# Performance work log

Measured on AMD Instinct MI355X. Metric: run time of the kernel, lower is better.

## Reference

```python
import jax, jax.numpy as jnp
import numpy as np
import math

B, C, H, W, S = 8, 512, 64, 64, 4


def setup_inputs() -> dict:
    key = jax.random.key(0)
    ks = jax.random.split(key, 7)
    s = 1.0 / math.sqrt(C)  # ~ torch Linear init scale
    x = jax.random.normal(ks[0], (B, C, H, W), jnp.float32)
    Wq = jax.random.uniform(ks[1], (C, C), jnp.float32, -s, s)
    bq = jax.random.uniform(ks[2], (C,), jnp.float32, -s, s)
    Wk = jax.random.uniform(ks[3], (C, C), jnp.float32, -s, s)
    bk = jax.random.uniform(ks[4], (C,), jnp.float32, -s, s)
    Wv = jax.random.uniform(ks[5], (C, C), jnp.float32, -s, s)
    bv = jax.random.uniform(ks[6], (C,), jnp.float32, -s, s)
    return {"x": x, "Wq": Wq, "bq": bq, "Wk": Wk, "bk": bk, "Wv": Wv, "bv": bv}


def reference(x, Wq, bq, Wk, bk, Wv, bv):
    # x: (B, C, H, W). Faithful to the torch module's output, but expressed
    # in the algebraically-equivalent efficient form: the repeat_interleaved
    # attention matrix A is block-constant, so out = repeat(A_m @ Vsum).
    b, c, h, w = x.shape
    nb = (h // S) * (w // S)  # number of SxS spatial blocks
    hw = h * w
    ss = S * S

    # Block means in unfold order (bh, bw): (B, nb, C)
    x_avg = x.reshape(b, c, h // S, S, w // S, S).mean(axis=(3, 5))
    x_avg = x_avg.reshape(b, c, nb).transpose(0, 2, 1)

    Q = x_avg @ Wq.T + bq  # (B, nb, C)
    K = x_avg @ Wk.T + bk  # (B, nb, C)
    A = jax.nn.softmax(jnp.einsum('bnc,bmc->bnm', Q, K) / jnp.sqrt(jnp.float32(c)), axis=-1)

    # V over flat row-major pixels: (B, HW, C)
    x_flat = x.reshape(b, c, hw).transpose(0, 2, 1)
    V = x_flat @ Wv.T + bv

    # repeat_interleave on dim=2 means column group j of A sums V rows
    # [j*ss, (j+1)*ss) in FLAT pixel order (not spatial blocks) - faithful.
    Vsum = V.reshape(b, hw // ss, ss, c).sum(axis=2)  # (B, nb, C)
    out_small = jnp.einsum('bnm,bmc->bnc', A, Vsum)   # (B, nb, C)
    # repeat_interleave on dim=1: each block row broadcast to ss flat pixels
    out_flat = jnp.repeat(out_small, ss, axis=1)      # (B, HW, C)
    return out_flat.transpose(0, 2, 1).reshape(b, c, h, w)
```

## Files before the change

kernel.cpp:

```cpp
#include <hip/hip_runtime.h>

typedef __attribute__((ext_vector_type(8))) short short8;
typedef __attribute__((ext_vector_type(4))) float f32x4;

__device__ __forceinline__ unsigned short f2bf(float f) {
    union { float f; unsigned int i; } v; v.f = f;
    unsigned int x = v.i;
    return (unsigned short)((x + 0x7FFFu + ((x >> 16) & 1u)) >> 16);
}
__device__ __forceinline__ f32x4 mfma16(short8 a, short8 b, f32x4 c) {
    return __builtin_amdgcn_mfma_f32_16x16x32_bf16(a, b, c, 0, 0, 0);
}

__global__ void prep_kernel(const float* __restrict__ x,
                            const float* __restrict__ Wq,
                            const float* __restrict__ Wk,
                            const float* __restrict__ Wv,
                            unsigned short* __restrict__ xavg,
                            unsigned short* __restrict__ xsum,
                            unsigned short* __restrict__ Wb)
{
    const int blk = blockIdx.x;
    const int t = threadIdx.x;
    if (blk >= 4096) {
        const int f = (blk - 4096) * 512 + t;
        const int m = f >> 16;
        const int o = f & 65535;
        const float4* s4 = (const float4*)((m == 0) ? Wq : (m == 1) ? Wk : Wv);
        float4 a = s4[o];
        float4 b = s4[o + 256];
        ushort4* d4 = (ushort4*)(Wb + (size_t)m * 262144);
        d4[o]       = make_ushort4(f2bf(a.x), f2bf(a.y), f2bf(a.z), f2bf(a.w));
        d4[o + 256] = make_ushort4(f2bf(b.x), f2bf(b.y), f2bf(b.z), f2bf(b.w));
        return;
    }
    const int b = blk >> 9;
    const int c = blk & 511;

    const float4* x4 = (const float4*)(x + (size_t)blk * 4096);
    float4 f0 = x4[t], f1 = x4[t + 256], f2 = x4[t + 512], f3 = x4[t + 768];

    __shared__ float part2[1024];
    part2[t]       = f0.x + f0.y + f0.z + f0.w;
    part2[t + 256] = f1.x + f1.y + f1.z + f1.w;
    part2[t + 512] = f2.x + f2.y + f2.z + f2.w;
    part2[t + 768] = f3.x + f3.y + f3.z + f3.w;
    __syncthreads();

    {
        const int base = 16 * (t >> 2) + 4 * (t & 3);
        float4 q = *(const float4*)&part2[base];
        xsum[((size_t)b * 256 + t) * 512 + c] = f2bf(q.x + q.y + q.z + q.w);
    }
    {
        const int bh = t >> 4, bw = t & 15;
        float m = (part2[(bh * 4 + 0) * 16 + bw] + part2[(bh * 4 + 1) * 16 + bw] +
                   part2[(bh * 4 + 2) * 16 + bw] + part2[(bh * 4 + 3) * 16 + bw]) * 0.0625f;
        xavg[((size_t)b * 256 + t) * 512 + c] = f2bf(m);
    }
}

__global__ void __launch_bounds__(256, 2)
proj_gemm(const unsigned short* __restrict__ xavg,
          const unsigned short* __restrict__ xsum,
          const unsigned short* __restrict__ Wb,
          const float* __restrict__ bq,
          const float* __restrict__ bk,
          const float* __restrict__ bv,
          unsigned short* __restrict__ QK,
          unsigned short* __restrict__ VsT)
{
    const int blk = blockIdx.x;
    const int lane = threadIdx.x & 63, quad = lane >> 4, r16 = lane & 15;
    const int w = threadIdx.x >> 6;

    if (blk < 256) {
        const int wave = blk * 4 + w;
        const int mt2 = wave >> 4;
        const int nt4 = wave & 15;
        const unsigned short* xp0 = xavg + (size_t)(mt2 * 32 + r16) * 512 + quad * 8;
        const unsigned short* xp1 = xp0 + 16 * 512;
        const unsigned short* wp0 = Wb + (size_t)(nt4 * 64 + r16) * 512 + quad * 8;
        const unsigned short* wp1 = wp0 + 16 * 512;
        const unsigned short* wp2 = wp0 + 32 * 512;
        const unsigned short* wp3 = wp0 + 48 * 512;

        f32x4 a00 = {0,0,0,0}, a01 = a00, a02 = a00, a03 = a00;
        f32x4 a10 = a00, a11 = a00, a12 = a00, a13 = a00;
#pragma unroll 4
        for (int k = 0; k < 512; k += 32) {
            short8 qa0 = *(const short8*)(xp0 + k);
            short8 qa1 = *(const short8*)(xp1 + k);
            short8 b0 = *(const short8*)(wp0 + k);
            short8 b1 = *(const short8*)(wp1 + k);
            short8 b2 = *(const short8*)(wp2 + k);
            short8 b3 = *(const short8*)(wp3 + k);
            a00 = mfma16(qa0, b0, a00); a01 = mfma16(qa0, b1, a01);
            a02 = mfma16(qa0, b2, a02); a03 = mfma16(qa0, b3, a03);
            a10 = mfma16(qa1, b0, a10); a11 = mfma16(qa1, b1, a11);
            a12 = mfma16(qa1, b2, a12); a13 = mfma16(qa1, b3, a13);
        }
        const int row0 = mt2 * 32 + quad * 4;
        f32x4 accs0[4] = {a00, a01, a02, a03};
        f32x4 accs1[4] = {a10, a11, a12, a13};
#pragma unroll
        for (int j = 0; j < 4; ++j) {
            const int c = nt4 * 64 + j * 16 + r16;
            const float bias = (c < 512) ? bq[c] : bk[c - 512];
#pragma unroll
            for (int r = 0; r < 4; ++r) {
                QK[(size_t)(row0 + r) * 1024 + c]      = f2bf(accs0[j][r] + bias);
                QK[(size_t)(row0 + 16 + r) * 1024 + c] = f2bf(accs1[j][r] + bias);
            }
        }
    } else {
        const int vblk = blk - 256;
        const int b = vblk >> 4;
        const int wave = (vblk & 15) * 4 + w;
        const int mt2 = wave >> 3;
        const int nt4 = wave & 7;
        const unsigned short* xp0 = xsum + (size_t)b * 131072 + (size_t)(mt2 * 32 + r16) * 512 + quad * 8;
        const unsigned short* xp1 = xp0 + 16 * 512;
        const unsigned short* wp0 = Wb + 524288 + (size_t)(nt4 * 64 + r16) * 512 + quad * 8;
        const unsigned short* wp1 = wp0 + 16 * 512;
        const unsigned short* wp2 = wp0 + 32 * 512;
        const unsigned short* wp3 = wp0 + 48 * 512;

        f32x4 a00 = {0,0,0,0}, a01 = a00, a02 = a00, a03 = a00;
        f32x4 a10 = a00, a11 = a00, a12 = a00, a13 = a00;
#pragma unroll 4
        for (int k = 0; k < 512; k += 32) {
            short8 qa0 = *(const short8*)(xp0 + k);
            short8 qa1 = *(const short8*)(xp1 + k);
            short8 b0 = *(const short8*)(wp0 + k);
            short8 b1 = *(const short8*)(wp1 + k);
            short8 b2 = *(const short8*)(wp2 + k);
            short8 b3 = *(const short8*)(wp3 + k);
            a00 = mfma16(qa0, b0, a00); a01 = mfma16(qa0, b1, a01);
            a02 = mfma16(qa0, b2, a02); a03 = mfma16(qa0, b3, a03);
            a10 = mfma16(qa1, b0, a10); a11 = mfma16(qa1, b1, a11);
            a12 = mfma16(qa1, b2, a12); a13 = mfma16(qa1, b3, a13);
        }
        unsigned short* vb = VsT + (size_t)b * 131072;
        const int m0 = mt2 * 32 + quad * 4;
        f32x4 accs0[4] = {a00, a01, a02, a03};
        f32x4 accs1[4] = {a10, a11, a12, a13};
#pragma unroll
        for (int j = 0; j < 4; ++j) {
            const int c = nt4 * 64 + j * 16 + r16;
            const float bias = 16.f * bv[c];
#pragma unroll
            for (int r = 0; r < 4; ++r) {
                vb[(size_t)c * 256 + m0 + r]      = f2bf(accs0[j][r] + bias);
                vb[(size_t)c * 256 + m0 + 16 + r] = f2bf(accs1[j][r] + bias);
            }
        }
    }
}

__global__ void __launch_bounds__(256, 2)
score_softmax(const unsigned short* __restrict__ QK,
              unsigned short* __restrict__ Amat)
{
    __shared__ float S[16][257];
    const int b = blockIdx.y, strip = blockIdx.x;
    const int w = threadIdx.x >> 6, lane = threadIdx.x & 63;
    const int quad = lane >> 4, r16 = lane & 15;

    {
        const unsigned short* qp = QK + (size_t)(b * 256 + strip * 16 + r16) * 1024 + quad * 8;
        const unsigned short* kp0 = QK + (size_t)(b * 256 + w * 64 + r16) * 1024 + 512 + quad * 8;
        const unsigned short* kp1 = kp0 + 16 * 1024;
        const unsigned short* kp2 = kp0 + 32 * 1024;
        const unsigned short* kp3 = kp0 + 48 * 1024;

        f32x4 a0 = {0,0,0,0}, a1 = a0, a2 = a0, a3 = a0;
#pragma unroll 4
        for (int k = 0; k < 512; k += 32) {
            short8 qa = *(const short8*)(qp + k);
            short8 b0 = *(const short8*)(kp0 + k);
            short8 b1 = *(const short8*)(kp1 + k);
            short8 b2 = *(const short8*)(kp2 + k);
            short8 b3 = *(const short8*)(kp3 + k);
            a0 = mfma16(qa, b0, a0); a1 = mfma16(qa, b1, a1);
            a2 = mfma16(qa, b2, a2); a3 = mfma16(qa, b3, a3);
        }
        f32x4 accs[4] = {a0, a1, a2, a3};
#pragma unroll
        for (int j = 0; j < 4; ++j) {
            const int col = w * 64 + j * 16 + r16;
#pragma unroll
            for (int r = 0; r < 4; ++r)
                S[quad * 4 + r][col] = accs[j][r];
        }
    }
    __syncthreads();

    {
        const int t = threadIdx.x;
        const int r = t >> 4, idx = t & 15;
        float v[16];
        float mx = -3.4e38f;
#pragma unroll
        for (int j = 0; j < 16; ++j) {
            v[j] = S[r][idx * 16 + j] * 0.044194173824159216f;
            mx = fmaxf(mx, v[j]);
        }
        mx = fmaxf(mx, __shfl_xor(mx, 1));
        mx = fmaxf(mx, __shfl_xor(mx, 2));
        mx = fmaxf(mx, __shfl_xor(mx, 4));
        mx = fmaxf(mx, __shfl_xor(mx, 8));
        float sum = 0.f;
#pragma unroll
        for (int j = 0; j < 16; ++j) { v[j] = __expf(v[j] - mx); sum += v[j]; }
        sum += __shfl_xor(sum, 1);
        sum += __shfl_xor(sum, 2);
        sum += __shfl_xor(sum, 4);
        sum += __shfl_xor(sum, 8);
        const float inv = 1.f / sum;
        unsigned short* ap = Amat + (size_t)b * 65536 + (size_t)(strip * 16 + r) * 256 + idx * 16;
#pragma unroll
        for (int j = 0; j < 16; j += 4)
            *(ushort4*)(ap + j) = make_ushort4(f2bf(v[j] * inv), f2bf(v[j + 1] * inv),
                                               f2bf(v[j + 2] * inv), f2bf(v[j + 3] * inv));
    }
}

__global__ void __launch_bounds__(256, 4)
av_expand(const unsigned short* __restrict__ Amat,
          const unsigned short* __restrict__ VsT,
          float* __restrict__ out)
{
    __shared__ float osT[64][17];
    const int b = blockIdx.y;
    const int sh = blockIdx.x >> 3;
    const int cq = blockIdx.x & 7;
    const int w = threadIdx.x >> 6, lane = threadIdx.x & 63;
    const int quad = lane >> 4, r16 = lane & 15;

    {
        const unsigned short* ap = Amat + (size_t)b * 65536 + (size_t)(sh * 16 + r16) * 256 + quad * 8;
        const unsigned short* vp = VsT + (size_t)b * 131072 +
                                   (size_t)(cq * 64 + w * 16 + r16) * 256 + quad * 8;
        f32x4 acc = {0.f, 0.f, 0.f, 0.f};
#pragma unroll
        for (int k = 0; k < 256; k += 32) {
            short8 a0 = *(const short8*)(ap + k);
            short8 b0 = *(const short8*)(vp + k);
            acc = mfma16(a0, b0, acc);
        }
#pragma unroll
        for (int r = 0; r < 4; ++r)
            osT[w * 16 + r16][quad * 4 + r] = acc[r];
    }
    __syncthreads();

    {
        const int t = threadIdx.x;
        const int ch4 = t >> 6;
        const int j = t & 63;
        const int n = j >> 2;
        float* obase = out + (size_t)(b * 512 + cq * 64) * 4096 + sh * 256 + j * 4;
#pragma unroll
        for (int it = 0; it < 16; ++it) {
            const int ch = it * 4 + ch4;
            const float v = osT[ch][n];
            *(float4*)(obase + (size_t)ch * 4096) = make_float4(v, v, v, v);
        }
    }
}

extern "C" void kernel_launch(void* const* d_in, const int* in_sizes, int n_in,
                              void* d_out, int out_size, void* d_ws, size_t ws_size,
                              hipStream_t stream) {
    const float* x  = (const float*)d_in[0];
    const float* Wq = (const float*)d_in[1];
    const float* bq = (const float*)d_in[2];
    const float* Wk = (const float*)d_in[3];
    const float* bk = (const float*)d_in[4];
    const float* Wv = (const float*)d_in[5];
    const float* bv = (const float*)d_in[6];
    float* out = (float*)d_out;

    unsigned short* Wb   = (unsigned short*)d_ws;
    unsigned short* xavg = Wb + 786432;
    unsigned short* xsum = xavg + 1048576;
    unsigned short* QK   = xsum + 1048576;
    unsigned short* VsT  = QK + 2097152;
    unsigned short* Amat = VsT + 1048576;

    prep_kernel<<<4480, 256, 0, stream>>>(x, Wq, Wk, Wv, xavg, xsum, Wb);
    proj_gemm<<<384, 256, 0, stream>>>(xavg, xsum, Wb, bq, bk, bv, QK, VsT);
    score_softmax<<<dim3(16, 8), 256, 0, stream>>>(QK, Amat);
    av_expand<<<dim3(128, 8), 256, 0, stream>>>(Amat, VsT, out);
}
```

Before: 180.4 us.

## Fuse score softmax and AV expansion into one kernel via shared-memory A

Merges the score/softmax kernel and the attention-times-V expansion kernel into one launch. The bf16 softmax rows stay in shared memory instead of making a round trip through global memory. Each block now covers a 16-row strip and half of the channels, so the QK score work is computed twice per strip. The output store is also restructured: each thread writes one channel row, rather than a wave writing contiguous spans, which may hurt store coalescing and lowers the number of blocks available for the large output write.

```diff
diff --git a/kernel.cpp b/kernel.cpp
--- a/kernel.cpp
+++ b/kernel.cpp
@@ -159,11 +159,19 @@
 }
 
 __global__ void __launch_bounds__(256, 2)
-score_softmax(const unsigned short* __restrict__ QK,
-              unsigned short* __restrict__ Amat)
+score_av(const unsigned short* __restrict__ QK,
+         const unsigned short* __restrict__ VsT,
+         float* __restrict__ out)
 {
-    __shared__ float S[16][257];
-    const int b = blockIdx.y, strip = blockIdx.x;
+    __shared__ union {
+        float S[16][257];
+        float osT[256][17];
+    } u;
+    __shared__ __align__(16) unsigned short Abf[16][264];
+
+    const int b = blockIdx.y;
+    const int strip = blockIdx.x >> 1;
+    const int chalf = blockIdx.x & 1;
     const int w = threadIdx.x >> 6, lane = threadIdx.x & 63;
     const int quad = lane >> 4, r16 = lane & 15;
 
@@ -191,7 +199,7 @@
             const int col = w * 64 + j * 16 + r16;
 #pragma unroll
             for (int r = 0; r < 4; ++r)
-                S[quad * 4 + r][col] = accs[j][r];
+                u.S[quad * 4 + r][col] = accs[j][r];
         }
     }
     __syncthreads();
@@ -203,7 +211,7 @@
         float mx = -3.4e38f;
 #pragma unroll
         for (int j = 0; j < 16; ++j) {
-            v[j] = S[r][idx * 16 + j] * 0.044194173824159216f;
+            v[j] = u.S[r][idx * 16 + j] * 0.044194173824159216f;
             mx = fmaxf(mx, v[j]);
         }
         mx = fmaxf(mx, __shfl_xor(mx, 1));
@@ -218,54 +226,56 @@
         sum += __shfl_xor(sum, 4);
         sum += __shfl_xor(sum, 8);
         const float inv = 1.f / sum;
-        unsigned short* ap = Amat + (size_t)b * 65536 + (size_t)(strip * 16 + r) * 256 + idx * 16;
+        unsigned short* ap = &Abf[r][idx * 16];
 #pragma unroll
         for (int j = 0; j < 16; j += 4)
             *(ushort4*)(ap + j) = make_ushort4(f2bf(v[j] * inv), f2bf(v[j + 1] * inv),
                                                f2bf(v[j + 2] * inv), f2bf(v[j + 3] * inv));
     }
-}
-
-__global__ void __launch_bounds__(256, 4)
-av_expand(const unsigned short* __restrict__ Amat,
-          const unsigned short* __restrict__ VsT,
-          float* __restrict__ out)
-{
-    __shared__ float osT[64][17];
-    const int b = blockIdx.y;
-    const int sh = blockIdx.x >> 3;
-    const int cq = blockIdx.x & 7;
-    const int w = threadIdx.x >> 6, lane = threadIdx.x & 63;
-    const int quad = lane >> 4, r16 = lane & 15;
-
-    {
-        const unsigned short* ap = Amat + (size_t)b * 65536 + (size_t)(sh * 16 + r16) * 256 + quad * 8;
-        const unsigned short* vp = VsT + (size_t)b * 131072 +
-                                   (size_t)(cq * 64 + w * 16 + r16) * 256 + quad * 8;
-        f32x4 acc = {0.f, 0.f, 0.f, 0.f};
-#pragma unroll
-        for (int k = 0; k < 256; k += 32) {
-            short8 a0 = *(const short8*)(ap + k);
-            short8 b0 = *(const short8*)(vp + k);
-            acc = mfma16(a0, b0, acc);
-        }
-#pragma unroll
-        for (int r = 0; r < 4; ++r)
-            osT[w * 16 + r16][quad * 4 + r] = acc[r];
-    }
     __syncthreads();
 
     {
+        f32x4 acc0 = {0,0,0,0}, acc1 = acc0, acc2 = acc0, acc3 = acc0;
+        const unsigned short* vbase = VsT + (size_t)b * 131072 +
+                                      (size_t)(chalf * 256 + w * 64 + r16) * 256 + quad * 8;
+        const unsigned short* vp0 = vbase;
+        const unsigned short* vp1 = vbase + 16 * 256;
+        const unsigned short* vp2 = vbase + 32 * 256;
+        const unsigned short* vp3 = vbase + 48 * 256;
+#pragma unroll
+        for (int kk = 0; kk < 256; kk += 32) {
+            short8 a = *(const short8*)(&Abf[r16][kk + quad * 8]);
+            short8 b0 = *(const short8*)(vp0 + kk);
+            short8 b1 = *(const short8*)(vp1 + kk);
+            short8 b2 = *(const short8*)(vp2 + kk);
+            short8 b3 = *(const short8*)(vp3 + kk);
+            acc0 = mfma16(a, b0, acc0); acc1 = mfma16(a, b1, acc1);
+            acc2 = mfma16(a, b2, acc2); acc3 = mfma16(a, b3, acc3);
+        }
+        __syncthreads();
+        f32x4 accs[4] = {acc0, acc1, acc2, acc3};
+#pragma unroll
+        for (int i = 0; i < 4; ++i) {
+            const int cl = w * 64 + i * 16 + r16;
+#pragma unroll
+            for (int r = 0; r < 4; ++r)
+                u.osT[cl][quad * 4 + r] = accs[i][r];
+        }
+    }
+    __syncthreads();
+
+    {
         const int t = threadIdx.x;
-        const int ch4 = t >> 6;
-        const int j = t & 63;
-        const int n = j >> 2;
-        float* obase = out + (size_t)(b * 512 + cq * 64) * 4096 + sh * 256 + j * 4;
-#pragma unroll
-        for (int it = 0; it < 16; ++it) {
-            const int ch = it * 4 + ch4;
-            const float v = osT[ch][n];
-            *(float4*)(obase + (size_t)ch * 4096) = make_float4(v, v, v, v);
+        const float* orow = &u.osT[t][0];
+        float* obase = out + (size_t)(b * 512 + chalf * 256 + t) * 4096 + strip * 256;
+#pragma unroll
+        for (int n = 0; n < 16; ++n) {
+            const float v = orow[n];
+            float4 v4 = make_float4(v, v, v, v);
+            *(float4*)(obase + n * 16)      = v4;
+            *(float4*)(obase + n * 16 + 4)  = v4;
+            *(float4*)(obase + n * 16 + 8)  = v4;
+            *(float4*)(obase + n * 16 + 12) = v4;
         }
     }
 }
@@ -287,10 +297,8 @@
     unsigned short* xsum = xavg + 1048576;
     unsigned short* QK   = xsum + 1048576;
     unsigned short* VsT  = QK + 2097152;
-    unsigned short* Amat = VsT + 1048576;
 
     prep_kernel<<<4480, 256, 0, stream>>>(x, Wq, Wk, Wv, xavg, xsum, Wb);
     proj_gemm<<<384, 256, 0, stream>>>(xavg, xsum, Wb, bq, bk, bv, QK, VsT);
-    score_softmax<<<dim3(16, 8), 256, 0, stream>>>(QK, Amat);
-    av_expand<<<dim3(128, 8), 256, 0, stream>>>(Amat, VsT, out);
-}
+    score_av<<<dim3(32, 8), 256, 0, stream>>>(QK, VsT, out);
+}
```

Result: slower. 185.0 us (+2.6%).
